# Kernel optimization log

Hardware: AMD Instinct MI355X
Metric: run time of the kernel (lower is better)

Reference implementation:

```python
import jax, jax.numpy as jnp
import numpy as np

B, S0, S1 = 4, 768, 256
T = S0 + S1
D0, D1 = 2048, 1024
N, K, H = 8, 1, 256  # num_heads, num_kv_heads, head_dim
G = N // K
BIG_NEG = -2.3819763e38


def _apply_rope(x, positions, max_wavelength=10000):
    # x: [B, L, Hn, Hd]; positions: [B, L] float32
    half = x.shape[-1] // 2
    freq_exponents = (2.0 / x.shape[-1]) * jnp.arange(half, dtype=jnp.float32)
    timescale = max_wavelength ** freq_exponents
    radians = positions[..., None] / timescale[None, None, :]   # [B, L, half]
    radians = radians[..., None, :]                             # [B, L, 1, half]
    sin, cos = jnp.sin(radians), jnp.cos(radians)
    x1, x2 = jnp.split(x, 2, axis=-1)
    res = jnp.concatenate([x1 * cos - x2 * sin, x2 * cos + x1 * sin], axis=-1)
    return res.astype(x.dtype)


def setup_inputs() -> dict:
    key = jax.random.key(0)
    ks = jax.random.split(key, 8)
    x0 = jax.random.normal(ks[0], (B, S0, D0), dtype=jnp.float32)
    x1 = jax.random.normal(ks[1], (B, S1, D1), dtype=jnp.float32)
    positions = jnp.broadcast_to(jnp.arange(T, dtype=jnp.float32), (B, T))
    # causal mask [B, 1, T, T]
    attn_mask = jnp.broadcast_to(jnp.tril(jnp.ones((T, T), dtype=bool)), (B, 1, T, T))
    # lecun_normal-style init: std = 1/sqrt(fan_in=width)
    q0_w = jax.random.normal(ks[2], (N, D0, H), dtype=jnp.float32) * (D0 ** -0.5)
    kv0_w = jax.random.normal(ks[3], (2, K, D0, H), dtype=jnp.float32) * (D0 ** -0.5)
    q1_w = jax.random.normal(ks[4], (N, D1, H), dtype=jnp.float32) * (D1 ** -0.5)
    kv1_w = jax.random.normal(ks[5], (2, K, D1, H), dtype=jnp.float32) * (D1 ** -0.5)
    o0_w = jax.random.normal(ks[6], (N, H, D0), dtype=jnp.float32) * ((N * H) ** -0.5)
    o1_w = jax.random.normal(ks[7], (N, H, D1), dtype=jnp.float32) * ((N * H) ** -0.5)
    return {"x0": x0, "x1": x1, "positions": positions, "attn_mask": attn_mask,
            "q0_w": q0_w, "kv0_w": kv0_w, "q1_w": q1_w, "kv1_w": kv1_w,
            "o0_w": o0_w, "o1_w": o1_w}


def reference(x0, x1, positions, attn_mask, q0_w, kv0_w, q1_w, kv1_w, o0_w, o1_w):
    dtype = x0.dtype
    # per-stream GQA projections (num_kv_heads != num_heads path)
    q_a = jnp.einsum('BTD,NDH->BTNH', x0, q0_w)
    kv_a = jnp.einsum('BSD,CKDH->CBSKH', x0, kv0_w)
    q_b = jnp.einsum('BTD,NDH->BTNH', x1, q1_w)
    kv_b = jnp.einsum('BSD,CKDH->CBSKH', x1, kv1_w)
    # concat streams along sequence
    q = jnp.concatenate([q_a, q_b], axis=1)                 # [B, T, N, H]
    k = jnp.concatenate([kv_a[0], kv_b[0]], axis=1)         # [B, T, K, H]
    v = jnp.concatenate([kv_a[1], kv_b[1]], axis=1)         # [B, T, K, H]
    # inline RoPE + query scaling
    q = _apply_rope(q, positions) * (H ** -0.5)
    k = _apply_rope(k, positions)
    # GQA grouping: N = K * G
    qg = q.reshape(q.shape[0], q.shape[1], K, G, H)          # [B, T, K, G, H]
    logits = jnp.einsum('BTKGH,BSKH->BKGTS', qg, k,
                        preferred_element_type=jnp.float32)  # fp32 scores
    masked = jnp.where(attn_mask[:, :, None, :, :], logits, BIG_NEG)
    probs = jax.nn.softmax(masked, axis=-1).astype(dtype)
    encoded = jnp.einsum('BKGTS,BSKH->BTKGH', probs, v)
    encoded = encoded.reshape(encoded.shape[0], encoded.shape[1], N, H)  # [B, T, N, H]
    out0 = jnp.einsum('BTNH,NHD->BTD', encoded[:, :S0], o0_w)
    out1 = jnp.einsum('BTNH,NHD->BTD', encoded[:, S0:], o1_w)
    return (out0, out1)
```

## Files before the change

### kernel.cpp

```cpp
#include <hip/hip_runtime.h>

typedef unsigned short u16;
typedef __attribute__((ext_vector_type(8))) short bf16x8;
typedef __attribute__((ext_vector_type(4))) float f32x4;

#define CB   4
#define CS0  768
#define CS1  256
#define CT   1024
#define CD0  2048
#define CD1  1024
#define CN   8
#define CH   256
#define IDENT (1 << 30)
#define BIGBASE 0x7fffffff

__device__ __forceinline__ float bf2f(u16 u) {
    union { unsigned int i; float f; } v;
    v.i = ((unsigned int)u) << 16;
    return v.f;
}
__device__ __forceinline__ u16 f2bf(float f) {
    union { float f; unsigned int i; } v;
    v.f = f;
    unsigned int r = 0x7fffu + ((v.i >> 16) & 1u);
    return (u16)((v.i + r) >> 16);
}

__device__ __forceinline__ void gl_lds16(const u16* g, u16* lds_base) {
    __builtin_amdgcn_global_load_lds(
        (const __attribute__((address_space(1))) void*)g,
        (__attribute__((address_space(3))) void*)lds_base,
        16, 0, 0);
}

struct PSeg { const float* in; u16* out; int R, C, base, lgx, lgy, mode; };
struct PSeg8 { PSeg t[8]; };

__global__ __launch_bounds__(256) void prep_multi(PSeg8 segs)
{
    __shared__ float tl[32][33];
    int bid = blockIdx.x;
    PSeg g = segs.t[0];
    #pragma unroll
    for (int i = 1; i < 8; i++)
        if (bid >= segs.t[i].base) g = segs.t[i];
    int r = bid - g.base;
    if (g.mode == 0) {
        int i = r * 256 + threadIdx.x;
        float4 v = ((const float4*)g.in)[i];
        ushort4 o;
        o.x = f2bf(v.x); o.y = f2bf(v.y); o.z = f2bf(v.z); o.w = f2bf(v.w);
        ((ushort4*)g.out)[i] = o;
    } else {
        int bx = r & ((1 << g.lgx) - 1);
        int by = (r >> g.lgx) & ((1 << g.lgy) - 1);
        int bz = r >> (g.lgx + g.lgy);
        const float* in = g.in + (size_t)bz * g.R * g.C;
        u16* out = g.out + (size_t)bz * g.R * g.C;
        int c0 = bx * 32, r0 = by * 32;
        int tx = threadIdx.x & 31, ty = threadIdx.x >> 5;
        #pragma unroll
        for (int i = 0; i < 32; i += 8)
            tl[ty + i][tx] = in[(size_t)(r0 + ty + i) * g.C + c0 + tx];
        __syncthreads();
        #pragma unroll
        for (int i = 0; i < 32; i += 8)
            out[(size_t)(c0 + ty + i) * g.R + r0 + tx] = f2bf(tl[tx][ty + i]);
    }
}

struct GSeg {
    const u16* A; const u16* BT; void* C;
    int K, Cstride, base, lgnx;
    int Sa, Ta, ta, Sc, Tc, tc, obf, pad;
};
struct GSeg4 { GSeg s[4]; };

__global__ __launch_bounds__(256) void mfma_gemm_multi(GSeg4 segs)
{
    __shared__ u16 As[128 * 32];
    __shared__ u16 Bs[128 * 32];

    int bid = blockIdx.x;
    GSeg g = segs.s[0];
    if (bid >= segs.s[1].base) g = segs.s[1];
    if (bid >= segs.s[2].base) g = segs.s[2];
    if (bid >= segs.s[3].base) g = segs.s[3];

    int tid  = threadIdx.x;
    int r    = bid - g.base;
    int n0   = (r & ((1 << g.lgnx) - 1)) * 128;
    int m0   = (r >> g.lgnx) * 128;
    int wave = tid >> 6, lane = tid & 63;

    int srow  = tid >> 2;
    int skoff = ((tid & 3) ^ ((srow >> 1) & 3)) * 8;
    int am1 = m0 + srow, am2 = m0 + 64 + srow;
    const u16* aptr1 = g.A + (size_t)((am1 / g.Sa) * g.Ta + g.ta + am1 % g.Sa) * g.K + skoff;
    const u16* aptr2 = g.A + (size_t)((am2 / g.Sa) * g.Ta + g.ta + am2 % g.Sa) * g.K + skoff;
    const u16* bptr1 = g.BT + (size_t)(n0 + srow) * g.K + skoff;
    const u16* bptr2 = g.BT + (size_t)(n0 + 64 + srow) * g.K + skoff;

    int mw = (wave >> 1) * 64, nw = (wave & 1) * 64;
    int lrow = lane & 15;
    int q4   = lane >> 4;
    int sw   = (q4 ^ ((lrow >> 1) & 3)) * 8;

    f32x4 acc[4][4] = {};

    for (int k0 = 0; k0 < g.K; k0 += 32) {
        gl_lds16(aptr1 + k0, As + wave * 512);
        gl_lds16(aptr2 + k0, As + 2048 + wave * 512);
        gl_lds16(bptr1 + k0, Bs + wave * 512);
        gl_lds16(bptr2 + k0, Bs + 2048 + wave * 512);
        __syncthreads();
        bf16x8 af[4], bfr[4];
        #pragma unroll
        for (int i = 0; i < 4; i++)
            af[i] = *(const bf16x8*)&As[(mw + i * 16 + lrow) * 32 + sw];
        #pragma unroll
        for (int i = 0; i < 4; i++)
            bfr[i] = *(const bf16x8*)&Bs[(nw + i * 16 + lrow) * 32 + sw];
        #pragma unroll
        for (int mi = 0; mi < 4; mi++)
            #pragma unroll
            for (int ni = 0; ni < 4; ni++)
                acc[mi][ni] = __builtin_amdgcn_mfma_f32_16x16x32_bf16(
                    af[mi], bfr[ni], acc[mi][ni], 0, 0, 0);
        __syncthreads();
    }

    #pragma unroll
    for (int mi = 0; mi < 4; mi++) {
        #pragma unroll
        for (int rr = 0; rr < 4; rr++) {
            int mm = m0 + mw + mi * 16 + q4 * 4 + rr;
            int grow = (mm / g.Sc) * g.Tc + g.tc + mm % g.Sc;
            if (g.obf) {
                u16* crow = (u16*)g.C + (size_t)grow * g.Cstride + n0 + nw + lrow;
                #pragma unroll
                for (int ni = 0; ni < 4; ni++)
                    crow[ni * 16] = f2bf(acc[mi][ni][rr]);
            } else {
                float* crow = (float*)g.C + (size_t)grow * g.Cstride + n0 + nw + lrow;
                #pragma unroll
                for (int ni = 0; ni < 4; ni++)
                    crow[ni * 16] = acc[mi][ni][rr];
            }
        }
    }
}

__global__ __launch_bounds__(256) void rope_vt_kernel(
    const u16* __restrict__ qsrc, const u16* __restrict__ kvsrc,
    const float* __restrict__ positions,
    u16* __restrict__ qb, u16* __restrict__ kb, u16* __restrict__ vto)
{
    int bid = blockIdx.x;
    if (bid < 18432) {
        int idx = bid * 256 + threadIdx.x;
        const int QP = CB * CT * CN * 128;
        if (idx < QP) {
            int h  = idx & 127;
            int n  = (idx >> 7) & 7;
            int bt = idx >> 10;
            const u16* base = qsrc + (size_t)bt * 2048 + n * 256;
            float pos = positions[bt];
            float ts  = powf(10000.0f, (float)h * (1.0f / 128.0f));
            float rr  = pos / ts;
            float sn = sinf(rr), cs = cosf(rr);
            float x1 = bf2f(base[h]), x2 = bf2f(base[h + 128]);
            u16* ob = qb + (size_t)bt * 2048 + n * 256;
            ob[h]       = f2bf((x1 * cs - x2 * sn) * 0.0625f);
            ob[h + 128] = f2bf((x2 * cs + x1 * sn) * 0.0625f);
        } else {
            int j  = idx - QP;
            int h  = j & 127;
            int bt = j >> 7;
            const u16* base = kvsrc + (size_t)bt * 512;
            float pos = positions[bt];
            float ts  = powf(10000.0f, (float)h * (1.0f / 128.0f));
            float rr  = pos / ts;
            float sn = sinf(rr), cs = cosf(rr);
            float x1 = bf2f(base[h]), x2 = bf2f(base[h + 128]);
            int b = bt >> 10, t = bt & 1023;
            int h2 = h + 128;
            kb[((size_t)(b * 8 + (h  >> 5)) * 1024 + t) * 32 + (h  & 31)] = f2bf(x1 * cs - x2 * sn);
            kb[((size_t)(b * 8 + (h2 >> 5)) * 1024 + t) * 32 + (h2 & 31)] = f2bf(x2 * cs + x1 * sn);
        }
    } else {
        int vb = bid - 18432;
        int h  = threadIdx.x;
        int sc = vb & 31;
        int b  = vb >> 5;
        const u16* src = kvsrc + ((size_t)(b * 1024 + sc * 32) * 512 + 256 + h);
        u16* dst = vto + ((size_t)(b * 32 + sc) * 256 + h) * 32;
        u16 buf[32];
        #pragma unroll
        for (int ss = 0; ss < 32; ss++)
            buf[ss] = src[(size_t)ss * 512];
        #pragma unroll
        for (int i = 0; i < 8; i++)
            ((ushort4*)dst)[i] = ((ushort4*)buf)[i];
    }
}

__global__ __launch_bounds__(256) void flash_attn(
    const u16* __restrict__ qb, const u16* __restrict__ kb,
    const u16* __restrict__ vt, u16* __restrict__ encoded)
{
    __shared__ __align__(16) u16 Ks[8 * 64 * 32];
    __shared__ __align__(16) u16 Vs[2 * 256 * 32];
    __shared__ __align__(16) u16 Pw[4][16 * 72];

    int tid  = threadIdx.x;
    int wave = tid >> 6, lane = tid & 63;
    int q4 = lane >> 4, l15 = lane & 15;
    int swz = (q4 ^ ((l15 >> 1) & 3)) * 8;

    int bid  = blockIdx.x;
    int half = bid >> 8;
    int r    = bid & 255;
    int b    = (half << 1) | (r >> 7);
    int ti   = r & 127;
    if (half) ti = 127 - ti;
    int t0 = ti * 8;

    bf16x8 af[8];
    {
        int m = wave * 16 + l15;
        int head = m >> 3, tl = m & 7;
        const u16* qrow = qb + ((size_t)(b * CT + t0 + tl) * 2048 + head * 256 + q4 * 8);
        #pragma unroll
        for (int kc = 0; kc < 8; kc++)
            af[kc] = *(const bf16x8*)(qrow + kc * 32);
    }

    f32x4 O[16] = {};
    float lrun[4] = {0.f, 0.f, 0.f, 0.f};

    int send = t0 + 8;
    for (int s0 = 0; s0 < send; s0 += 64) {
        bool lastTile = (s0 + 64 >= send);
        if (s0) __syncthreads();
        #pragma unroll
        for (int is = 0; is < 8; is++) {
            int ubase = is * 256 + wave * 64;
            int u = ubase + lane;
            int s = (u >> 2) & 63, hc = u >> 8;
            int ug = (u & 3) ^ ((s >> 1) & 3);
            const u16* g = kb + ((size_t)((b * 8 + hc) * 1024 + s0 + s) * 32 + ug * 8);
            gl_lds16(g, Ks + (size_t)ubase * 8);
        }
        #pragma unroll
        for (int is = 0; is < 8; is++) {
            int ubase = is * 256 + wave * 64;
            int u = ubase + lane;
            int h = (u >> 2) & 255;
            int vg = (u & 3) ^ ((h >> 1) & 3);
            const u16* g = vt + ((size_t)(b * 32 + (s0 >> 5)) * 8192 + (size_t)(u >> 2) * 32 + vg * 8);
            gl_lds16(g, Vs + (size_t)ubase * 8);
        }
        __syncthreads();

        f32x4 P[4];
        #pragma unroll
        for (int ni = 0; ni < 4; ni++) {
            f32x4 c = {};
            #pragma unroll
            for (int kc = 0; kc < 8; kc++) {
                bf16x8 bfr = *(const bf16x8*)&Ks[kc * 2048 + (ni * 16 + l15) * 32 + swz];
                c = __builtin_amdgcn_mfma_f32_16x16x32_bf16(af[kc], bfr, c, 0, 0, 0);
            }
            P[ni] = c;
        }

        if (lastTile) {
            #pragma unroll
            for (int ni = 0; ni < 4; ni++)
                #pragma unroll
                for (int rr = 0; rr < 4; rr++) {
                    int trow = t0 + ((q4 * 4 + rr) & 7);
                    int scol = s0 + ni * 16 + l15;
                    if (scol > trow) P[ni][rr] = -3.0e38f;
                }
        }

        #pragma unroll
        for (int ni = 0; ni < 4; ni++)
            #pragma unroll
            for (int rr = 0; rr < 4; rr++) {
                float e = __expf(P[ni][rr]);
                P[ni][rr] = e;
                Pw[wave][(q4 * 4 + rr) * 72 + ni * 16 + l15] = f2bf(e);
            }
        #pragma unroll
        for (int rr = 0; rr < 4; rr++) {
            float s = (P[0][rr] + P[1][rr]) + (P[2][rr] + P[3][rr]);
            s += __shfl_xor(s, 1);
            s += __shfl_xor(s, 2);
            s += __shfl_xor(s, 4);
            s += __shfl_xor(s, 8);
            lrun[rr] += s;
        }

        bf16x8 pa0 = *(const bf16x8*)&Pw[wave][l15 * 72 + q4 * 8];
        bf16x8 pa1 = *(const bf16x8*)&Pw[wave][l15 * 72 + 32 + q4 * 8];
        #pragma unroll
        for (int nc = 0; nc < 16; nc++) {
            bf16x8 b0 = *(const bf16x8*)&Vs[(nc * 16 + l15) * 32 + swz];
            bf16x8 b1 = *(const bf16x8*)&Vs[8192 + (nc * 16 + l15) * 32 + swz];
            O[nc] = __builtin_amdgcn_mfma_f32_16x16x32_bf16(pa0, b0, O[nc], 0, 0, 0);
            O[nc] = __builtin_amdgcn_mfma_f32_16x16x32_bf16(pa1, b1, O[nc], 0, 0, 0);
        }
    }

    #pragma unroll
    for (int rr = 0; rr < 4; rr++) {
        int mm = wave * 16 + q4 * 4 + rr;
        int hd = mm >> 3, tl = mm & 7;
        u16* erow = encoded + ((size_t)(b * CT + t0 + tl) * 2048 + hd * 256 + l15);
        float inv = 1.0f / lrun[rr];
        #pragma unroll
        for (int nc = 0; nc < 16; nc++)
            erow[nc * 16] = f2bf(O[nc][rr] * inv);
    }
}

extern "C" void kernel_launch(void* const* d_in, const int* in_sizes, int n_in,
                              void* d_out, int out_size, void* d_ws, size_t ws_size,
                              hipStream_t stream)
{
    const float* x0        = (const float*)d_in[0];
    const float* x1        = (const float*)d_in[1];
    const float* positions = (const float*)d_in[2];
    const float* q0_w  = (const float*)d_in[4];
    const float* kv0_w = (const float*)d_in[5];
    const float* q1_w  = (const float*)d_in[6];
    const float* kv1_w = (const float*)d_in[7];
    const float* o0_w  = (const float*)d_in[8];
    const float* o1_w  = (const float*)d_in[9];
    float* out = (float*)d_out;

    char* W = (char*)d_ws;
    u16* qbuf16  = (u16*)(W);
    u16* kvbuf16 = (u16*)(W + 16777216);
    u16* WTo0  = (u16*)(W + 20971520);
    u16* WTo1  = (u16*)(W + 29360128);
    u16* x0b   = (u16*)(W + 33554432);
    u16* x1b   = (u16*)(W + 46137344);
    u16* WTq0  = (u16*)(W + 48234496);
    u16* WTkv0 = (u16*)(W + 56623104);
    u16* WTq1  = (u16*)(W + 58720256);
    u16* WTkv1 = (u16*)(W + 62914560);
    u16* qb  = x0b;
    u16* kb  = WTkv0;
    u16* vtb = WTq1;
    u16* encoded = qbuf16;

    PSeg8 ps8;
    ps8.t[0] = { x0,    x0b,      0,    0,     0, 0, 0, 0 };
    ps8.t[1] = { x1,    x1b,      0,    0,  6144, 0, 0, 0 };
    ps8.t[2] = { q0_w,  WTq0,  2048,  256,  7168, 3, 6, 1 };
    ps8.t[3] = { kv0_w, WTkv0, 2048,  256, 11264, 3, 6, 1 };
    ps8.t[4] = { q1_w,  WTq1,  1024,  256, 12288, 3, 5, 1 };
    ps8.t[5] = { kv1_w, WTkv1, 1024,  256, 14336, 3, 5, 1 };
    ps8.t[6] = { o0_w,  WTo0,  2048, 2048, 14848, 6, 6, 1 };
    ps8.t[7] = { o1_w,  WTo1,  2048, 1024, 18944, 5, 6, 1 };
    prep_multi<<<dim3(20992), dim3(256), 0, stream>>>(ps8);

    GSeg4 ps;
    ps.s[0] = { x0b, WTq0,  qbuf16,  2048, 2048,   0, 4, IDENT, 0, 0, CS0, CT, 0,   1, 0 };
    ps.s[1] = { x0b, WTkv0, kvbuf16, 2048,  512, 384, 2, IDENT, 0, 0, CS0, CT, 0,   1, 0 };
    ps.s[2] = { x1b, WTq1,  qbuf16,  1024, 2048, 480, 4, IDENT, 0, 0, CS1, CT, CS0, 1, 0 };
    ps.s[3] = { x1b, WTkv1, kvbuf16, 1024,  512, 608, 2, IDENT, 0, 0, CS1, CT, CS0, 1, 0 };
    mfma_gemm_multi<<<dim3(640), dim3(256), 0, stream>>>(ps);

    rope_vt_kernel<<<dim3(18560), dim3(256), 0, stream>>>(
        qbuf16, kvbuf16, positions, qb, kb, vtb);

    flash_attn<<<dim3(512), dim3(256), 0, stream>>>(qb, kb, vtb, encoded);

    GSeg4 os;
    os.s[0] = { encoded, WTo0, out, 2048, 2048,   0, 4, CS0, CT, 0,   IDENT, 0, 0, 0, 0 };
    os.s[1] = { encoded, WTo1, out + (size_t)CB * CS0 * CD0,
                2048, 1024, 384, 3, CS1, CT, CS0, IDENT, 0, 0, 0, 0 };
    os.s[2] = { nullptr, nullptr, nullptr, 0, 0, BIGBASE, 0, 1, 0, 0, 1, 0, 0, 0, 0 };
    os.s[3] = { nullptr, nullptr, nullptr, 0, 0, BIGBASE, 0, 1, 0, 0, 1, 0, 0, 0, 0 };
    mfma_gemm_multi<<<dim3(448), dim3(256), 0, stream>>>(os);
}
```

Before: 331.2 us.

## Replace 128x128 GEMM with 256x256 tiles and 4-stage async LDS pipeline

Replaces the 128x128-tile, 256-thread GEMM with a 256x256-tile, 512-thread kernel that keeps four k-slices in dynamic LDS. Loads are issued three stages ahead, with explicit vmcnt waits and barriers between the halves of the MFMA work. The change targets the synchronous load-then-compute stall of the old loop and aims for more reuse per tile. In exchange the projection grids shrink to 160 and 112 blocks, which may underfill the GPU, and each block now needs 128KB of LDS.

```diff
diff --git a/kernel.cpp b/kernel.cpp
--- a/kernel.cpp
+++ b/kernel.cpp
@@ -77,10 +77,9 @@
 };
 struct GSeg4 { GSeg s[4]; };
 
-__global__ __launch_bounds__(256) void mfma_gemm_multi(GSeg4 segs)
+__global__ __launch_bounds__(512, 2) void gemm256_multi(GSeg4 segs)
 {
-    __shared__ u16 As[128 * 32];
-    __shared__ u16 Bs[128 * 32];
+    extern __shared__ __align__(16) u16 lds[];
 
     int bid = blockIdx.x;
     GSeg g = segs.s[0];
@@ -90,63 +89,94 @@
 
     int tid  = threadIdx.x;
     int r    = bid - g.base;
-    int n0   = (r & ((1 << g.lgnx) - 1)) * 128;
-    int m0   = (r >> g.lgnx) * 128;
+    int n0   = (r & ((1 << g.lgnx) - 1)) * 256;
+    int m0   = (r >> g.lgnx) * 256;
     int wave = tid >> 6, lane = tid & 63;
+    int wr   = wave >> 2, wc = wave & 3;
 
     int srow  = tid >> 2;
     int skoff = ((tid & 3) ^ ((srow >> 1) & 3)) * 8;
-    int am1 = m0 + srow, am2 = m0 + 64 + srow;
+    int am0 = m0 + srow, am1 = m0 + 128 + srow;
+    const u16* aptr0 = g.A + (size_t)((am0 / g.Sa) * g.Ta + g.ta + am0 % g.Sa) * g.K + skoff;
     const u16* aptr1 = g.A + (size_t)((am1 / g.Sa) * g.Ta + g.ta + am1 % g.Sa) * g.K + skoff;
-    const u16* aptr2 = g.A + (size_t)((am2 / g.Sa) * g.Ta + g.ta + am2 % g.Sa) * g.K + skoff;
-    const u16* bptr1 = g.BT + (size_t)(n0 + srow) * g.K + skoff;
-    const u16* bptr2 = g.BT + (size_t)(n0 + 64 + srow) * g.K + skoff;
-
-    int mw = (wave >> 1) * 64, nw = (wave & 1) * 64;
-    int lrow = lane & 15;
-    int q4   = lane >> 4;
-    int sw   = (q4 ^ ((lrow >> 1) & 3)) * 8;
-
-    f32x4 acc[4][4] = {};
-
-    for (int k0 = 0; k0 < g.K; k0 += 32) {
-        gl_lds16(aptr1 + k0, As + wave * 512);
-        gl_lds16(aptr2 + k0, As + 2048 + wave * 512);
-        gl_lds16(bptr1 + k0, Bs + wave * 512);
-        gl_lds16(bptr2 + k0, Bs + 2048 + wave * 512);
-        __syncthreads();
-        bf16x8 af[4], bfr[4];
-        #pragma unroll
-        for (int i = 0; i < 4; i++)
-            af[i] = *(const bf16x8*)&As[(mw + i * 16 + lrow) * 32 + sw];
-        #pragma unroll
-        for (int i = 0; i < 4; i++)
-            bfr[i] = *(const bf16x8*)&Bs[(nw + i * 16 + lrow) * 32 + sw];
-        #pragma unroll
-        for (int mi = 0; mi < 4; mi++)
-            #pragma unroll
-            for (int ni = 0; ni < 4; ni++)
-                acc[mi][ni] = __builtin_amdgcn_mfma_f32_16x16x32_bf16(
-                    af[mi], bfr[ni], acc[mi][ni], 0, 0, 0);
-        __syncthreads();
-    }
+    const u16* bptr0 = g.BT + (size_t)(n0 + srow) * g.K + skoff;
+    const u16* bptr1 = g.BT + (size_t)(n0 + 128 + srow) * g.K + skoff;
+
+    int l15 = lane & 15, q4 = lane >> 4;
+    int swz = (q4 ^ ((l15 >> 1) & 3)) * 8;
+
+#define STAGE_A(tt) do { int kk = (tt) * 32; \
+        u16* d = lds + ((tt) & 3) * 16384 + tid * 8; \
+        gl_lds16(aptr0 + kk, d); gl_lds16(aptr1 + kk, d + 4096); } while (0)
+#define STAGE_B(tt) do { int kk = (tt) * 32; \
+        u16* d = lds + ((tt) & 3) * 16384 + 8192 + tid * 8; \
+        gl_lds16(bptr0 + kk, d); gl_lds16(bptr1 + kk, d + 4096); } while (0)
+
+    f32x4 acc[8][4] = {};
+    int nkt = g.K >> 5;
+
+    STAGE_A(0); STAGE_B(0);
+    STAGE_A(1); STAGE_B(1);
+    STAGE_A(2); STAGE_B(2);
+
+    for (int t = 0; t < nkt; ++t) {
+        if (t + 2 < nkt)      asm volatile("s_waitcnt vmcnt(8)" ::: "memory");
+        else if (t + 1 < nkt) asm volatile("s_waitcnt vmcnt(4)" ::: "memory");
+        else                  asm volatile("s_waitcnt vmcnt(0)" ::: "memory");
+        __builtin_amdgcn_sched_barrier(0);
+        __builtin_amdgcn_s_barrier();
+        asm volatile("" ::: "memory");
+
+        const u16* At = lds + (t & 3) * 16384;
+        const u16* Bt = At + 8192;
+
+        bf16x8 af[8], bf0, bf1;
+        #pragma unroll
+        for (int m = 0; m < 8; ++m)
+            af[m] = *(const bf16x8*)&At[(wr * 128 + m * 16 + l15) * 32 + swz];
+        bf0 = *(const bf16x8*)&Bt[(wc * 64 +  0 + l15) * 32 + swz];
+        bf1 = *(const bf16x8*)&Bt[(wc * 64 + 16 + l15) * 32 + swz];
+        if (t + 3 < nkt) STAGE_A(t + 3);
+        __builtin_amdgcn_s_barrier();
+        __builtin_amdgcn_s_setprio(1);
+        #pragma unroll
+        for (int m = 0; m < 8; ++m) {
+            acc[m][0] = __builtin_amdgcn_mfma_f32_16x16x32_bf16(af[m], bf0, acc[m][0], 0, 0, 0);
+            acc[m][1] = __builtin_amdgcn_mfma_f32_16x16x32_bf16(af[m], bf1, acc[m][1], 0, 0, 0);
+        }
+        __builtin_amdgcn_s_setprio(0);
+
+        bf16x8 bg0 = *(const bf16x8*)&Bt[(wc * 64 + 32 + l15) * 32 + swz];
+        bf16x8 bg1 = *(const bf16x8*)&Bt[(wc * 64 + 48 + l15) * 32 + swz];
+        if (t + 3 < nkt) STAGE_B(t + 3);
+        __builtin_amdgcn_s_barrier();
+        __builtin_amdgcn_s_setprio(1);
+        #pragma unroll
+        for (int m = 0; m < 8; ++m) {
+            acc[m][2] = __builtin_amdgcn_mfma_f32_16x16x32_bf16(af[m], bg0, acc[m][2], 0, 0, 0);
+            acc[m][3] = __builtin_amdgcn_mfma_f32_16x16x32_bf16(af[m], bg1, acc[m][3], 0, 0, 0);
+        }
+        __builtin_amdgcn_s_setprio(0);
+    }
+#undef STAGE_A
+#undef STAGE_B
 
     #pragma unroll
-    for (int mi = 0; mi < 4; mi++) {
-        #pragma unroll
-        for (int rr = 0; rr < 4; rr++) {
-            int mm = m0 + mw + mi * 16 + q4 * 4 + rr;
+    for (int m = 0; m < 8; ++m) {
+        #pragma unroll
+        for (int rr = 0; rr < 4; ++rr) {
+            int mm = m0 + wr * 128 + m * 16 + q4 * 4 + rr;
             int grow = (mm / g.Sc) * g.Tc + g.tc + mm % g.Sc;
             if (g.obf) {
-                u16* crow = (u16*)g.C + (size_t)grow * g.Cstride + n0 + nw + lrow;
+                u16* crow = (u16*)g.C + (size_t)grow * g.Cstride + n0 + wc * 64 + l15;
                 #pragma unroll
-                for (int ni = 0; ni < 4; ni++)
-                    crow[ni * 16] = f2bf(acc[mi][ni][rr]);
+                for (int n = 0; n < 4; ++n)
+                    crow[n * 16] = f2bf(acc[m][n][rr]);
             } else {
-                float* crow = (float*)g.C + (size_t)grow * g.Cstride + n0 + nw + lrow;
+                float* crow = (float*)g.C + (size_t)grow * g.Cstride + n0 + wc * 64 + l15;
                 #pragma unroll
-                for (int ni = 0; ni < 4; ni++)
-                    crow[ni * 16] = acc[mi][ni][rr];
+                for (int n = 0; n < 4; ++n)
+                    crow[n * 16] = acc[m][n][rr];
             }
         }
     }
@@ -343,6 +373,13 @@
     const float* o1_w  = (const float*)d_in[9];
     float* out = (float*)d_out;
 
+    static int attr_done = 0;
+    if (!attr_done) {
+        hipFuncSetAttribute((const void*)gemm256_multi,
+                            hipFuncAttributeMaxDynamicSharedMemorySize, 131072);
+        attr_done = 1;
+    }
+
     char* W = (char*)d_ws;
     u16* qbuf16  = (u16*)(W);
     u16* kvbuf16 = (u16*)(W + 16777216);
@@ -371,11 +408,11 @@
     prep_multi<<<dim3(20992), dim3(256), 0, stream>>>(ps8);
 
     GSeg4 ps;
-    ps.s[0] = { x0b, WTq0,  qbuf16,  2048, 2048,   0, 4, IDENT, 0, 0, CS0, CT, 0,   1, 0 };
-    ps.s[1] = { x0b, WTkv0, kvbuf16, 2048,  512, 384, 2, IDENT, 0, 0, CS0, CT, 0,   1, 0 };
-    ps.s[2] = { x1b, WTq1,  qbuf16,  1024, 2048, 480, 4, IDENT, 0, 0, CS1, CT, CS0, 1, 0 };
-    ps.s[3] = { x1b, WTkv1, kvbuf16, 1024,  512, 608, 2, IDENT, 0, 0, CS1, CT, CS0, 1, 0 };
-    mfma_gemm_multi<<<dim3(640), dim3(256), 0, stream>>>(ps);
+    ps.s[0] = { x0b, WTq0,  qbuf16,  2048, 2048,   0, 3, IDENT, 0, 0, CS0, CT, 0,   1, 0 };
+    ps.s[1] = { x0b, WTkv0, kvbuf16, 2048,  512,  96, 1, IDENT, 0, 0, CS0, CT, 0,   1, 0 };
+    ps.s[2] = { x1b, WTq1,  qbuf16,  1024, 2048, 120, 3, IDENT, 0, 0, CS1, CT, CS0, 1, 0 };
+    ps.s[3] = { x1b, WTkv1, kvbuf16, 1024,  512, 152, 1, IDENT, 0, 0, CS1, CT, CS0, 1, 0 };
+    gemm256_multi<<<dim3(160), dim3(512), 131072, stream>>>(ps);
 
     rope_vt_kernel<<<dim3(18560), dim3(256), 0, stream>>>(
         qbuf16, kvbuf16, positions, qb, kb, vtb);
@@ -383,10 +420,10 @@
     flash_attn<<<dim3(512), dim3(256), 0, stream>>>(qb, kb, vtb, encoded);
 
     GSeg4 os;
-    os.s[0] = { encoded, WTo0, out, 2048, 2048,   0, 4, CS0, CT, 0,   IDENT, 0, 0, 0, 0 };
+    os.s[0] = { encoded, WTo0, out, 2048, 2048, 0, 3, CS0, CT, 0, IDENT, 0, 0, 0, 0 };
     os.s[1] = { encoded, WTo1, out + (size_t)CB * CS0 * CD0,
-                2048, 1024, 384, 3, CS1, CT, CS0, IDENT, 0, 0, 0, 0 };
-    os.s[2] = { nullptr, nullptr, nullptr, 0, 0, BIGBASE, 0, 1, 0, 0, 1, 0, 0, 0, 0 };
-    os.s[3] = { nullptr, nullptr, nullptr, 0, 0, BIGBASE, 0, 1, 0, 0, 1, 0, 0, 0, 0 };
-    mfma_gemm_multi<<<dim3(448), dim3(256), 0, stream>>>(os);
-}
+                2048, 1024, 96, 2, CS1, CT, CS0, IDENT, 0, 0, 0, 0 };
+    os.s[2] = { nullptr, nullptr, nullptr, 32, 0, BIGBASE, 0, 1, 0, 0, 1, 0, 0, 0, 0 };
+    os.s[3] = { nullptr, nullptr, nullptr, 32, 0, BIGBASE, 0, 1, 0, 0, 1, 0, 0, 0, 0 };
+    gemm256_multi<<<dim3(112), dim3(512), 131072, stream>>>(os);
+}
```

Measured after the change: 328.7 us. About the same (-0.7%).

## Double-buffer LDS in multi-segment GEMM to overlap global loads with MFMA

Applied to the files above, without the earlier changes.

Rewrites the 128x128 bf16 MFMA GEMM used for the QKV and output projections to use two LDS stages. The next K-tile is issued with direct-to-LDS loads while the current tile is computed, which cuts the per-iteration barrier count from two to one. It also raises wave priority around the MFMA block and adds a launch-bounds occupancy hint. In exchange, LDS use doubles to 32 KB per block, which may limit how many blocks fit per CU, and the explicit vmcnt(0) wait still serialises on the prefetch each iteration.

```diff
diff --git a/kernel.cpp b/kernel.cpp
--- a/kernel.cpp
+++ b/kernel.cpp
@@ -77,10 +77,9 @@
 };
 struct GSeg4 { GSeg s[4]; };
 
-__global__ __launch_bounds__(256) void mfma_gemm_multi(GSeg4 segs)
+__global__ __launch_bounds__(256, 3) void gemm128_multi(GSeg4 segs)
 {
-    __shared__ u16 As[128 * 32];
-    __shared__ u16 Bs[128 * 32];
+    __shared__ __align__(16) u16 lds[2 * 8192];
 
     int bid = blockIdx.x;
     GSeg g = segs.s[0];
@@ -103,33 +102,50 @@
     const u16* bptr2 = g.BT + (size_t)(n0 + 64 + srow) * g.K + skoff;
 
     int mw = (wave >> 1) * 64, nw = (wave & 1) * 64;
-    int lrow = lane & 15;
-    int q4   = lane >> 4;
-    int sw   = (q4 ^ ((lrow >> 1) & 3)) * 8;
+    int l15 = lane & 15;
+    int q4  = lane >> 4;
+    int sw  = (q4 ^ ((l15 >> 1) & 3)) * 8;
+
+#define STAGE(tt) do { int kk = (tt) * 32; \
+        u16* base = lds + ((tt) & 1) * 8192 + wave * 512; \
+        gl_lds16(aptr1 + kk, base); \
+        gl_lds16(aptr2 + kk, base + 2048); \
+        gl_lds16(bptr1 + kk, base + 4096); \
+        gl_lds16(bptr2 + kk, base + 6144); } while (0)
 
     f32x4 acc[4][4] = {};
-
-    for (int k0 = 0; k0 < g.K; k0 += 32) {
-        gl_lds16(aptr1 + k0, As + wave * 512);
-        gl_lds16(aptr2 + k0, As + 2048 + wave * 512);
-        gl_lds16(bptr1 + k0, Bs + wave * 512);
-        gl_lds16(bptr2 + k0, Bs + 2048 + wave * 512);
-        __syncthreads();
+    int nkt = g.K >> 5;
+
+    STAGE(0);
+
+    for (int t = 0; t < nkt; ++t) {
+        asm volatile("s_waitcnt vmcnt(0)" ::: "memory");
+        __builtin_amdgcn_sched_barrier(0);
+        __builtin_amdgcn_s_barrier();
+        asm volatile("" ::: "memory");
+        if (t + 1 < nkt) STAGE(t + 1);
+
+        const u16* At = lds + (t & 1) * 8192;
+        const u16* Bt = At + 4096;
         bf16x8 af[4], bfr[4];
         #pragma unroll
         for (int i = 0; i < 4; i++)
-            af[i] = *(const bf16x8*)&As[(mw + i * 16 + lrow) * 32 + sw];
+            af[i] = *(const bf16x8*)&At[(mw + i * 16 + l15) * 32 + sw];
         #pragma unroll
         for (int i = 0; i < 4; i++)
-            bfr[i] = *(const bf16x8*)&Bs[(nw + i * 16 + lrow) * 32 + sw];
+            bfr[i] = *(const bf16x8*)&Bt[(nw + i * 16 + l15) * 32 + sw];
+        asm volatile("s_waitcnt lgkmcnt(0)" ::: "memory");
+        __builtin_amdgcn_sched_barrier(0);
+        __builtin_amdgcn_s_setprio(1);
         #pragma unroll
         for (int mi = 0; mi < 4; mi++)
             #pragma unroll
             for (int ni = 0; ni < 4; ni++)
                 acc[mi][ni] = __builtin_amdgcn_mfma_f32_16x16x32_bf16(
                     af[mi], bfr[ni], acc[mi][ni], 0, 0, 0);
-        __syncthreads();
-    }
+        __builtin_amdgcn_s_setprio(0);
+    }
+#undef STAGE
 
     #pragma unroll
     for (int mi = 0; mi < 4; mi++) {
@@ -138,12 +154,12 @@
             int mm = m0 + mw + mi * 16 + q4 * 4 + rr;
             int grow = (mm / g.Sc) * g.Tc + g.tc + mm % g.Sc;
             if (g.obf) {
-                u16* crow = (u16*)g.C + (size_t)grow * g.Cstride + n0 + nw + lrow;
+                u16* crow = (u16*)g.C + (size_t)grow * g.Cstride + n0 + nw + l15;
                 #pragma unroll
                 for (int ni = 0; ni < 4; ni++)
                     crow[ni * 16] = f2bf(acc[mi][ni][rr]);
             } else {
-                float* crow = (float*)g.C + (size_t)grow * g.Cstride + n0 + nw + lrow;
+                float* crow = (float*)g.C + (size_t)grow * g.Cstride + n0 + nw + l15;
                 #pragma unroll
                 for (int ni = 0; ni < 4; ni++)
                     crow[ni * 16] = acc[mi][ni][rr];
@@ -375,7 +391,7 @@
     ps.s[1] = { x0b, WTkv0, kvbuf16, 2048,  512, 384, 2, IDENT, 0, 0, CS0, CT, 0,   1, 0 };
     ps.s[2] = { x1b, WTq1,  qbuf16,  1024, 2048, 480, 4, IDENT, 0, 0, CS1, CT, CS0, 1, 0 };
     ps.s[3] = { x1b, WTkv1, kvbuf16, 1024,  512, 608, 2, IDENT, 0, 0, CS1, CT, CS0, 1, 0 };
-    mfma_gemm_multi<<<dim3(640), dim3(256), 0, stream>>>(ps);
+    gemm128_multi<<<dim3(640), dim3(256), 0, stream>>>(ps);
 
     rope_vt_kernel<<<dim3(18560), dim3(256), 0, stream>>>(
         qbuf16, kvbuf16, positions, qb, kb, vtb);
@@ -386,7 +402,7 @@
     os.s[0] = { encoded, WTo0, out, 2048, 2048,   0, 4, CS0, CT, 0,   IDENT, 0, 0, 0, 0 };
     os.s[1] = { encoded, WTo1, out + (size_t)CB * CS0 * CD0,
                 2048, 1024, 384, 3, CS1, CT, CS0, IDENT, 0, 0, 0, 0 };
-    os.s[2] = { nullptr, nullptr, nullptr, 0, 0, BIGBASE, 0, 1, 0, 0, 1, 0, 0, 0, 0 };
-    os.s[3] = { nullptr, nullptr, nullptr, 0, 0, BIGBASE, 0, 1, 0, 0, 1, 0, 0, 0, 0 };
-    mfma_gemm_multi<<<dim3(448), dim3(256), 0, stream>>>(os);
-}
+    os.s[2] = { nullptr, nullptr, nullptr, 32, 0, BIGBASE, 0, 1, 0, 0, 1, 0, 0, 0, 0 };
+    os.s[3] = { nullptr, nullptr, nullptr, 32, 0, BIGBASE, 0, 1, 0, 0, 1, 0, 0, 0, 0 };
+    gemm128_multi<<<dim3(448), dim3(256), 0, stream>>>(os);
+}
```

Measured after the change: 308.9 us. 1.07x faster.
